# Optimization experiments

Measured on AMD Instinct MI355X. Metric: run time of the kernel, lower is better.

Reference implementation:

```python
import jax, jax.numpy as jnp
import numpy as np

VOCAB = 50257
N_EMBD = 640
BLOCK = 256
B = 16


def setup_inputs() -> dict:
    key = jax.random.key(0)
    ks = jax.random.split(key, 8)
    std = 0.02
    return {
        "idx": jax.random.randint(ks[0], (B, BLOCK), 0, VOCAB, dtype=jnp.int64 if jax.config.jax_enable_x64 else jnp.int32),
        "w_embed": jax.random.normal(ks[1], (VOCAB, N_EMBD), jnp.float32) * std,
        "w_pos": jax.random.normal(ks[2], (BLOCK, N_EMBD), jnp.float32) * std,
        "wq": jax.random.normal(ks[3], (N_EMBD, N_EMBD), jnp.float32) * std,
        "wk": jax.random.normal(ks[4], (N_EMBD, N_EMBD), jnp.float32) * std,
        "wv": jax.random.normal(ks[5], (N_EMBD, N_EMBD), jnp.float32) * std,
        "w_out": jax.random.normal(ks[6], (VOCAB, N_EMBD), jnp.float32) * std,
        "b_out": jnp.zeros((VOCAB,), jnp.float32),
    }


def reference(idx, w_embed, w_pos, wq, wk, wv, w_out, b_out):
    # idx: (B, T) token ids. Dropout is identity (eval mode).
    Bt, T = idx.shape
    x = w_embed[idx] + w_pos[:T]                      # (B, T, D)
    q = jnp.einsum('btd,ed->bte', x, wq)              # torch Linear: x @ W.T
    k = jnp.einsum('btd,ed->bte', x, wk)
    v = jnp.einsum('btd,ed->bte', x, wv)
    scale = jnp.asarray(N_EMBD ** 0.5, x.dtype)
    scores = jnp.einsum('btd,bsd->bts', q, k) / scale  # (B, T, T)
    causal = jnp.triu(jnp.ones((T, T), bool), k=1)     # True above diagonal
    scores = jnp.where(causal, jnp.asarray(-jnp.inf, scores.dtype), scores)
    attn = jax.nn.softmax(scores, axis=-1)
    attn_out = jnp.einsum('bts,bsd->btd', attn, v)     # (B, T, D)
    logits = jnp.einsum('btd,vd->btv', attn_out, w_out) + b_out  # (B, T, V)
    return logits
```

## Files before the change

### kernel.cpp

```cpp
#include <hip/hip_runtime.h>
#include <hip/hip_bf16.h>
#include <stdint.h>

#define VOCAB 50257
#define VPAD  50432
#define DIM   640
#define SEQ   256
#define NBATCH 16
#define MROWS 4096

using bf16 = __hip_bfloat16;
typedef __attribute__((ext_vector_type(8))) short short8;
typedef __attribute__((ext_vector_type(4))) float f32x4;
struct bf16x4 { bf16 a, b, c, d; };

__device__ __forceinline__ void gld_lds16(const void* g, void* l) {
  __builtin_amdgcn_global_load_lds(
      (const __attribute__((address_space(1))) void*)g,
      (__attribute__((address_space(3))) void*)l, 16, 0, 0);
}

#define BAR() asm volatile("s_barrier" ::: "memory")
#define VMC(n) asm volatile("s_waitcnt vmcnt(" #n ")" ::: "memory")

__global__ void embed_kernel(const int* __restrict__ idx,
                             const float* __restrict__ we,
                             const float* __restrict__ wp,
                             bf16* __restrict__ xb) {
  int row = blockIdx.x;
  int t = row & (SEQ - 1);
  int tok = idx[row];
  const float* src = we + (long)tok * DIM;
  const float* pos = wp + (long)t * DIM;
  for (int d = threadIdx.x * 4; d < DIM; d += blockDim.x * 4) {
    float4 s = *(const float4*)(src + d);
    float4 p = *(const float4*)(pos + d);
    bf16x4 o = { __float2bfloat16(s.x + p.x), __float2bfloat16(s.y + p.y),
                 __float2bfloat16(s.z + p.z), __float2bfloat16(s.w + p.w) };
    *(bf16x4*)(xb + (long)row * DIM + d) = o;
  }
}

__global__ void conv4_kernel(const float* __restrict__ src, bf16* __restrict__ dst,
                             long n_src, long n_dst) {
  long i = ((long)blockIdx.x * blockDim.x + threadIdx.x) * 4;
  long stride = (long)gridDim.x * blockDim.x * 4;
  for (; i < n_dst; i += stride) {
    float4 v = (i < n_src) ? *(const float4*)(src + i) : make_float4(0.f, 0.f, 0.f, 0.f);
    bf16x4 o = { __float2bfloat16(v.x), __float2bfloat16(v.y),
                 __float2bfloat16(v.z), __float2bfloat16(v.w) };
    *(bf16x4*)(dst + i) = o;
  }
}

__global__ void transpose_v(const bf16* __restrict__ v, bf16* __restrict__ vt) {
  long i = (long)blockIdx.x * blockDim.x + threadIdx.x;
  if (i >= (long)NBATCH * DIM * SEQ) return;
  int t = (int)(i & (SEQ - 1));
  long be = i >> 8;
  int e = (int)(be % DIM);
  int b = (int)(be / DIM);
  vt[i] = v[((long)b * SEQ + t) * DIM + e];
}

__global__ void softmax_kernel(const float* __restrict__ sc, bf16* __restrict__ p) {
  int wid = threadIdx.x >> 6, lane = threadIdx.x & 63;
  int row = blockIdx.x * 4 + wid;
  int t = row & (SEQ - 1);
  const float* srow = sc + (long)row * SEQ;
  const float rsc = 0.03952847075210474f;
  float v[4];
  float mx = -1e30f;
#pragma unroll
  for (int i = 0; i < 4; ++i) {
    int s = lane + 64 * i;
    v[i] = (s <= t) ? srow[s] * rsc : -1e30f;
    mx = fmaxf(mx, v[i]);
  }
#pragma unroll
  for (int off = 32; off; off >>= 1) mx = fmaxf(mx, __shfl_xor(mx, off, 64));
  float sum = 0.f;
#pragma unroll
  for (int i = 0; i < 4; ++i) {
    int s = lane + 64 * i;
    v[i] = (s <= t) ? __expf(v[i] - mx) : 0.f;
    sum += v[i];
  }
#pragma unroll
  for (int off = 32; off; off >>= 1) sum += __shfl_xor(sum, off, 64);
  float inv = 1.f / sum;
#pragma unroll
  for (int i = 0; i < 4; ++i)
    p[(long)row * SEQ + lane + 64 * i] = __float2bfloat16(v[i] * inv);
}

template <int NT, typename OUT_T, bool BIAS>
__global__ __launch_bounds__(256, 3) void gemm_pipe(
    const bf16* __restrict__ Ag, const bf16* __restrict__ Bg,
    OUT_T* __restrict__ Cg, const float* __restrict__ bias,
    int K, int ldc, int Nstore, long sA, long sB, long sC) {
  __shared__ __align__(16) char lds[49152];
  const int tid = threadIdx.x;
  const int lane = tid & 63, wv = tid >> 6;
  const int lr = lane & 15, h16 = lane >> 4;

  const int tm = blockIdx.x, tn = blockIdx.y, bz = blockIdx.z;
  const bf16* A = Ag + (long)bz * sA + (long)tm * 128 * K;
  const bf16* B = Bg + (long)bz * sB + (long)tn * 128 * K;

  int srcE[2], dstW[2];
#pragma unroll
  for (int j = 0; j < 2; ++j) {
    int d = j * 256 + tid;
    int b = d ^ ((d >> 3) & 3);
    srcE[j] = (b >> 2) * K + (b & 3) * 8;
    dstW[j] = (j * 256 + wv * 64) * 16;
  }
  const bf16* aS0 = A + srcE[0];
  const bf16* aS1 = A + srcE[1];
  const bf16* bS0 = B + srcE[0];
  const bf16* bS1 = B + srcE[1];
  auto STAGE = [&](int slot, int t) {
    int kOff = t * 32;
    gld_lds16(aS0 + kOff, lds + slot + dstW[0]);
    gld_lds16(aS1 + kOff, lds + slot + dstW[1]);
    gld_lds16(bS0 + kOff, lds + slot + 8192 + dstW[0]);
    gld_lds16(bS1 + kOff, lds + slot + 8192 + dstW[1]);
  };

  const int wr = (wv >> 1) * 64, wc = (wv & 1) * 64;
  int aoff[4], boff[4];
#pragma unroll
  for (int m = 0; m < 4; ++m) {
    int La = (wr + m * 16 + lr) * 64 + h16 * 16;
    aoff[m] = La ^ (((La >> 7) & 3) << 4);
    int Lb = (wc + m * 16 + lr) * 64 + h16 * 16;
    boff[m] = 8192 + (Lb ^ (((Lb >> 7) & 3) << 4));
  }

  f32x4 acc[4][4] = {};
  short8 a[4], b[4];

  STAGE(0, 0);
  if (NT > 1) STAGE(16384, 1);
  VMC(4);
  BAR();

#pragma unroll
  for (int t = 0; t < NT; ++t) {
    const int cur = (t % 3) * 16384;
    if (t + 2 < NT) STAGE(((t + 2) % 3) * 16384, t + 2);
#pragma unroll
    for (int m = 0; m < 4; ++m) a[m] = *(const short8*)(lds + cur + aoff[m]);
#pragma unroll
    for (int n = 0; n < 4; ++n) b[n] = *(const short8*)(lds + cur + boff[n]);
    __builtin_amdgcn_s_setprio(1);
#pragma unroll
    for (int m = 0; m < 4; ++m)
#pragma unroll
      for (int n = 0; n < 4; ++n)
        acc[m][n] = __builtin_amdgcn_mfma_f32_16x16x32_bf16(a[m], b[n], acc[m][n], 0, 0, 0);
    __builtin_amdgcn_s_setprio(0);
    if (t + 2 < NT) { VMC(4); }
    else if (t + 1 < NT) { VMC(0); }
    BAR();
  }

  if constexpr (sizeof(OUT_T) == 4) {
    float* Cf = (float*)Cg + (long)bz * sC;
    float bv[4];
#pragma unroll
    for (int n = 0; n < 4; ++n) {
      int col = tn * 128 + wc + lr + n * 16;
      bv[n] = (BIAS && col < Nstore) ? bias[col] : 0.f;
    }
    char* reg = lds + wv * 8192;
    const int rowL = lane & 31, cb = lane >> 5;
#pragma unroll
    for (int mm = 0; mm < 2; ++mm) {
#pragma unroll
      for (int mp = 0; mp < 2; ++mp)
#pragma unroll
        for (int n = 0; n < 4; ++n) {
          f32x4 v = acc[mm * 2 + mp][n];
          v[0] += bv[n]; v[1] += bv[n]; v[2] += bv[n]; v[3] += bv[n];
          int col = lr + n * 16;
          int rho = mp * 16 + h16 * 4;
          int w = col * 32 + (rho ^ ((col & 7) << 2));
          *(f32x4*)(reg + w * 4) = v;
        }
      const long rowg = tm * 128 + wr + mm * 32 + rowL;
#pragma unroll
      for (int k = 0; k < 8; ++k) {
        f32x4 o;
#pragma unroll
        for (int c = 0; c < 4; ++c) {
          int col = k * 8 + cb * 4 + c;
          int w = col * 32 + (rowL ^ ((col & 7) << 2));
          o[c] = *(const float*)(reg + w * 4);
        }
        int gcol = tn * 128 + wc + k * 8 + cb * 4;
        if (gcol + 3 < Nstore) {
          *(f32x4*)(Cf + rowg * (long)ldc + gcol) = o;
        } else {
#pragma unroll
          for (int c = 0; c < 4; ++c)
            if (gcol + c < Nstore) Cf[rowg * (long)ldc + gcol + c] = o[c];
        }
      }
    }
  } else {
    OUT_T* C = Cg + (long)bz * sC;
    const int crow0 = tm * 128 + wr + h16 * 4;
    const int ccol0 = tn * 128 + wc + lr;
#pragma unroll
    for (int m = 0; m < 4; ++m)
#pragma unroll
      for (int n = 0; n < 4; ++n) {
        int col = ccol0 + n * 16;
        if (col < Nstore) {
#pragma unroll
          for (int j = 0; j < 4; ++j) {
            long row = crow0 + m * 16 + j;
            C[row * ldc + col] = __float2bfloat16(acc[m][n][j]);
          }
        }
      }
  }
}

extern "C" void kernel_launch(void* const* d_in, const int* in_sizes, int n_in,
                              void* d_out, int out_size, void* d_ws, size_t ws_size,
                              hipStream_t stream) {
  const int*   idx     = (const int*)d_in[0];
  const float* w_embed = (const float*)d_in[1];
  const float* w_pos   = (const float*)d_in[2];
  const float* wq      = (const float*)d_in[3];
  const float* wk      = (const float*)d_in[4];
  const float* wv      = (const float*)d_in[5];
  const float* w_out   = (const float*)d_in[6];
  const float* b_out   = (const float*)d_in[7];
  float* out = (float*)d_out;

  size_t off = 0;
  auto alloc = [&](size_t bytes) {
    void* p = (char*)d_ws + off;
    off += (bytes + 255) & ~(size_t)255;
    return p;
  };
  bf16* x_bf    = (bf16*)alloc((size_t)MROWS * DIM * 2);
  bf16* wqkv_bf = (bf16*)alloc((size_t)3 * DIM * DIM * 2);
  bf16* wout_bf = (bf16*)alloc((size_t)VPAD * DIM * 2);
  bf16* qkv     = (bf16*)alloc((size_t)3 * MROWS * DIM * 2);
  bf16* vT      = (bf16*)alloc((size_t)NBATCH * DIM * SEQ * 2);
  float* scores = (float*)alloc((size_t)NBATCH * SEQ * SEQ * 4);
  bf16* P       = (bf16*)alloc((size_t)NBATCH * SEQ * SEQ * 2);
  bf16* attn    = (bf16*)alloc((size_t)MROWS * DIM * 2);

  const long QKV_S = (long)MROWS * DIM;
  const long W_S   = (long)DIM * DIM;

  embed_kernel<<<MROWS, 256, 0, stream>>>(idx, w_embed, w_pos, x_bf);

  conv4_kernel<<<256, 256, 0, stream>>>(wq, wqkv_bf,           W_S, W_S);
  conv4_kernel<<<256, 256, 0, stream>>>(wk, wqkv_bf + W_S,     W_S, W_S);
  conv4_kernel<<<256, 256, 0, stream>>>(wv, wqkv_bf + 2 * W_S, W_S, W_S);
  conv4_kernel<<<2048, 256, 0, stream>>>(w_out, wout_bf, (long)VOCAB * DIM, (long)VPAD * DIM);

  gemm_pipe<20, bf16, false><<<dim3(MROWS / 128, DIM / 128, 3), 256, 0, stream>>>(
      x_bf, wqkv_bf, qkv, nullptr, DIM, DIM, DIM, 0, W_S, QKV_S);

  {
    long n = (long)NBATCH * DIM * SEQ;
    transpose_v<<<(int)((n + 255) / 256), 256, 0, stream>>>(qkv + 2 * QKV_S, vT);
  }

  gemm_pipe<20, float, false><<<dim3(SEQ / 128, SEQ / 128, NBATCH), 256, 0, stream>>>(
      qkv, qkv + QKV_S, scores, nullptr, DIM, SEQ, SEQ,
      (long)SEQ * DIM, (long)SEQ * DIM, (long)SEQ * SEQ);

  softmax_kernel<<<MROWS / 4, 256, 0, stream>>>(scores, P);

  gemm_pipe<8, bf16, false><<<dim3(SEQ / 128, DIM / 128, NBATCH), 256, 0, stream>>>(
      P, vT, attn, nullptr, SEQ, DIM, DIM,
      (long)SEQ * SEQ, (long)DIM * SEQ, (long)SEQ * DIM);

  gemm_pipe<20, float, true><<<dim3(MROWS / 128, VPAD / 128, 1), 256, 0, stream>>>(
      attn, wout_bf, out, b_out, DIM, VOCAB, VOCAB, 0, 0, 0);
}
```

Measured before the change: 635.7 us.

## Switch GEMM to double-buffered LDS for higher occupancy, nontemporal logits stores

The GEMM pipeline drops from a 3-stage to a 2-stage LDS ring, which cuts shared memory from 48KB to 32KB and raises launch bounds to 4 blocks per CU. The goal is more resident waves to hide latency. The trade-off is less prefetch depth: each iteration now waits for vmcnt(0) before the barrier. The final vocab-projection GEMM also writes its large fp32 logits output with nontemporal stores, to reduce cache pollution from the write stream.

```diff
diff --git a/kernel.cpp b/kernel.cpp
--- a/kernel.cpp
+++ b/kernel.cpp
@@ -21,7 +21,7 @@
 }
 
 #define BAR() asm volatile("s_barrier" ::: "memory")
-#define VMC(n) asm volatile("s_waitcnt vmcnt(" #n ")" ::: "memory")
+#define VMC0() asm volatile("s_waitcnt vmcnt(0)" ::: "memory")
 
 __global__ void embed_kernel(const int* __restrict__ idx,
                              const float* __restrict__ we,
@@ -94,12 +94,12 @@
     p[(long)row * SEQ + lane + 64 * i] = __float2bfloat16(v[i] * inv);
 }
 
-template <int NT, typename OUT_T, bool BIAS>
-__global__ __launch_bounds__(256, 3) void gemm_pipe(
+template <int NT, typename OUT_T, bool BIAS, bool NTS>
+__global__ __launch_bounds__(256, 4) void gemm_pipe(
     const bf16* __restrict__ Ag, const bf16* __restrict__ Bg,
     OUT_T* __restrict__ Cg, const float* __restrict__ bias,
     int K, int ldc, int Nstore, long sA, long sB, long sC) {
-  __shared__ __align__(16) char lds[49152];
+  __shared__ __align__(16) char lds[32768];
   const int tid = threadIdx.x;
   const int lane = tid & 63, wv = tid >> 6;
   const int lr = lane & 15, h16 = lane >> 4;
@@ -142,14 +142,13 @@
   short8 a[4], b[4];
 
   STAGE(0, 0);
-  if (NT > 1) STAGE(16384, 1);
-  VMC(4);
+  VMC0();
   BAR();
 
-#pragma unroll
+#pragma unroll 2
   for (int t = 0; t < NT; ++t) {
-    const int cur = (t % 3) * 16384;
-    if (t + 2 < NT) STAGE(((t + 2) % 3) * 16384, t + 2);
+    const int cur = (t & 1) * 16384;
+    if (t + 1 < NT) STAGE(16384 - cur, t + 1);
 #pragma unroll
     for (int m = 0; m < 4; ++m) a[m] = *(const short8*)(lds + cur + aoff[m]);
 #pragma unroll
@@ -161,8 +160,7 @@
       for (int n = 0; n < 4; ++n)
         acc[m][n] = __builtin_amdgcn_mfma_f32_16x16x32_bf16(a[m], b[n], acc[m][n], 0, 0, 0);
     __builtin_amdgcn_s_setprio(0);
-    if (t + 2 < NT) { VMC(4); }
-    else if (t + 1 < NT) { VMC(0); }
+    if (t + 1 < NT) VMC0();
     BAR();
   }
 
@@ -200,12 +198,17 @@
           o[c] = *(const float*)(reg + w * 4);
         }
         int gcol = tn * 128 + wc + k * 8 + cb * 4;
+        float* dst = Cf + rowg * (long)ldc + gcol;
         if (gcol + 3 < Nstore) {
-          *(f32x4*)(Cf + rowg * (long)ldc + gcol) = o;
+          if constexpr (NTS) __builtin_nontemporal_store(o, (f32x4*)dst);
+          else               *(f32x4*)dst = o;
         } else {
 #pragma unroll
           for (int c = 0; c < 4; ++c)
-            if (gcol + c < Nstore) Cf[rowg * (long)ldc + gcol + c] = o[c];
+            if (gcol + c < Nstore) {
+              if constexpr (NTS) __builtin_nontemporal_store(o[c], dst + c);
+              else               dst[c] = o[c];
+            }
         }
       }
     }
@@ -267,7 +270,7 @@
   conv4_kernel<<<256, 256, 0, stream>>>(wv, wqkv_bf + 2 * W_S, W_S, W_S);
   conv4_kernel<<<2048, 256, 0, stream>>>(w_out, wout_bf, (long)VOCAB * DIM, (long)VPAD * DIM);
 
-  gemm_pipe<20, bf16, false><<<dim3(MROWS / 128, DIM / 128, 3), 256, 0, stream>>>(
+  gemm_pipe<20, bf16, false, false><<<dim3(MROWS / 128, DIM / 128, 3), 256, 0, stream>>>(
       x_bf, wqkv_bf, qkv, nullptr, DIM, DIM, DIM, 0, W_S, QKV_S);
 
   {
@@ -275,16 +278,16 @@
     transpose_v<<<(int)((n + 255) / 256), 256, 0, stream>>>(qkv + 2 * QKV_S, vT);
   }
 
-  gemm_pipe<20, float, false><<<dim3(SEQ / 128, SEQ / 128, NBATCH), 256, 0, stream>>>(
+  gemm_pipe<20, float, false, false><<<dim3(SEQ / 128, SEQ / 128, NBATCH), 256, 0, stream>>>(
       qkv, qkv + QKV_S, scores, nullptr, DIM, SEQ, SEQ,
       (long)SEQ * DIM, (long)SEQ * DIM, (long)SEQ * SEQ);
 
   softmax_kernel<<<MROWS / 4, 256, 0, stream>>>(scores, P);
 
-  gemm_pipe<8, bf16, false><<<dim3(SEQ / 128, DIM / 128, NBATCH), 256, 0, stream>>>(
+  gemm_pipe<8, bf16, false, false><<<dim3(SEQ / 128, DIM / 128, NBATCH), 256, 0, stream>>>(
       P, vT, attn, nullptr, SEQ, DIM, DIM,
       (long)SEQ * SEQ, (long)DIM * SEQ, (long)SEQ * DIM);
 
-  gemm_pipe<20, float, true><<<dim3(MROWS / 128, VPAD / 128, 1), 256, 0, stream>>>(
+  gemm_pipe<20, float, true, true><<<dim3(MROWS / 128, VPAD / 128, 1), 256, 0, stream>>>(
       attn, wout_bf, out, b_out, DIM, VOCAB, VOCAB, 0, 0, 0);
 }
```

New measurement: 1.679 ms. +164.1%, slower.
